# Performance work log

Measured on AMD Instinct MI355X. Metric: run time of the kernel, lower is better.

Reference implementation:

```python
import jax, jax.numpy as jnp
import numpy as np

EMB = 1024
HEADS = 16
RATE = 1.0


def setup_inputs() -> dict:
    key = jax.random.key(0)
    ks = jax.random.split(key, 11)
    B, S, D = 2, 2048, EMB
    s = 1.0 / np.sqrt(D)
    inp = {
        "q": jax.random.normal(ks[0], (B, S, D), jnp.float32),
        "k": jax.random.normal(ks[1], (B, S, D), jnp.float32),
        "v": jax.random.normal(ks[2], (B, S, D), jnp.float32),
        "Wq": jax.random.normal(ks[3], (D, D), jnp.float32) * s,
        "bq": jnp.zeros((D,), jnp.float32),
        "Wk": jax.random.normal(ks[4], (D, D), jnp.float32) * s,
        "bk": jnp.zeros((D,), jnp.float32),
        "Wv": jax.random.normal(ks[5], (D, D), jnp.float32) * s,
        "bv": jnp.zeros((D,), jnp.float32),
        "Wo": jax.random.normal(ks[6], (D, D), jnp.float32) * s,
        "bo": jnp.zeros((D,), jnp.float32),
    }
    return inp


def _mha(q, k, v, Wq, bq, Wk, bk, Wv, bv, Wo, bo):
    B, S, D = q.shape
    H = HEADS
    hd = D // H
    temp = jnp.asarray(hd ** 0.5, q.dtype)

    def proj(x, W, b):
        # nn.Linear: x @ W.T + b, then Scaler: /rate
        y = (jnp.einsum('bsd,ed->bse', x, W) + b) / RATE
        # [B,S,D] -> [B,H,S,hd]
        return y.reshape(B, S, H, hd).transpose(0, 2, 1, 3)

    qh, kh, vh = proj(q, Wq, bq), proj(k, Wk, bk), proj(v, Wv, bv)
    scores = jnp.einsum('bhqd,bhkd->bhqk', qh, kh) / temp  # [B,H,S,S]
    causal = jnp.tril(jnp.ones((S, S), bool))
    scores = jnp.where(causal, scores, jnp.asarray(-jnp.inf, scores.dtype))
    attn = jax.nn.softmax(scores, axis=-1)
    out = jnp.einsum('bhqk,bhkd->bhqd', attn, vh)  # [B,H,S,hd]
    out = out.transpose(0, 2, 1, 3).reshape(B, S, D)
    out = (jnp.einsum('bsd,ed->bse', out, Wo) + bo) / RATE
    # attn returned as [B*H, S, S] to match torch reshape-to-batches layout
    return out, attn.reshape(B * H, S, S)


def reference(q, k, v, Wq, bq, Wk, bk, Wv, bv, Wo, bo):
    return _mha(q, k, v, Wq, bq, Wk, bk, Wv, bv, Wo, bo)
```

## Files before the change

kernel.cpp:

```cpp
#include <hip/hip_runtime.h>
#include <hip/hip_bf16.h>
#include <stdint.h>


#define SLEN 2048
#define DMODEL 1024
#define NBH 32

typedef __bf16 bf16x8 __attribute__((ext_vector_type(8)));
typedef float f32x4 __attribute__((ext_vector_type(4)));
typedef unsigned short us8 __attribute__((ext_vector_type(8)));

__device__ __forceinline__ unsigned short f2bf(float f) {
  union { float f; uint32_t u; } x; x.f = f;
  uint32_t r = x.u + 0x7fffu + ((x.u >> 16) & 1u);
  return (unsigned short)(r >> 16);
}

__device__ __forceinline__ f32x4 mfma16(us8 a, us8 b, f32x4 c) {
  return __builtin_amdgcn_mfma_f32_16x16x32_bf16(
      __builtin_bit_cast(bf16x8, a), __builtin_bit_cast(bf16x8, b), c, 0, 0, 0);
}

__device__ __forceinline__ void gld16(void* lds, const void* g) {
  __builtin_amdgcn_global_load_lds(
      (__attribute__((address_space(1))) void*)(g),
      (__attribute__((address_space(3))) void*)(lds), 16, 0, 0);
}

__device__ __forceinline__ int sw8(int r, int c)  { return (r * 8  + (c ^ (r & 7)))  * 16; }
__device__ __forceinline__ int sw16(int r, int c) { return (r * 16 + (c ^ (r & 15))) * 16; }

__global__ __launch_bounds__(256)
void convert_bf16(const float* __restrict__ q, const float* __restrict__ k,
                  const float* __restrict__ v, const float* __restrict__ wq,
                  const float* __restrict__ wk, const float* __restrict__ wv,
                  const float* __restrict__ wo, unsigned short* __restrict__ dst) {
  size_t i = ((size_t)blockIdx.x * 256 + threadIdx.x) * 8;
  const float* src;
  size_t off;
  if      (i <  4194304u) { src = q;  off = i; }
  else if (i <  8388608u) { src = k;  off = i -  4194304u; }
  else if (i < 12582912u) { src = v;  off = i -  8388608u; }
  else if (i < 13631488u) { src = wq; off = i - 12582912u; }
  else if (i < 14680064u) { src = wk; off = i - 13631488u; }
  else if (i < 15728640u) { src = wv; off = i - 14680064u; }
  else                    { src = wo; off = i - 15728640u; }
  float4 a = *(const float4*)(src + off);
  float4 b = *(const float4*)(src + off + 4);
  us8 u;
  u[0]=f2bf(a.x); u[1]=f2bf(a.y); u[2]=f2bf(a.z); u[3]=f2bf(a.w);
  u[4]=f2bf(b.x); u[5]=f2bf(b.y); u[6]=f2bf(b.z); u[7]=f2bf(b.w);
  *(us8*)(dst + i) = u;
}

__global__ __launch_bounds__(256)
void gemm_qkv_bf(const unsigned short* __restrict__ xq, const unsigned short* __restrict__ xk,
                 const unsigned short* __restrict__ xv, const unsigned short* __restrict__ wwq,
                 const unsigned short* __restrict__ wwk, const unsigned short* __restrict__ wwv,
                 const float* __restrict__ bbq, const float* __restrict__ bbk,
                 const float* __restrict__ bbv,
                 unsigned short* __restrict__ qh, unsigned short* __restrict__ kk,
                 unsigned short* __restrict__ vt) {
  __shared__ __align__(16) unsigned char As[16384];
  __shared__ __align__(16) unsigned char Bs[16384];
  const int p = blockIdx.z;
  const unsigned short* X = (p == 0) ? xq  : (p == 1) ? xk  : xv;
  const unsigned short* W = (p == 0) ? wwq : (p == 1) ? wwk : wwv;
  const float* bias       = (p == 0) ? bbq : (p == 1) ? bbk : bbv;
  const int n0 = blockIdx.x * 128, m0 = blockIdx.y * 128;
  const int t = threadIdx.x, lane = t & 63, w = t >> 6;
  const int quad = lane >> 4, l16 = lane & 15;
  const int wm = w >> 1, wn = w & 1;
  f32x4 acc[4][4] = {};

  for (int kt = 0; kt < 16; ++kt) {
#pragma unroll
    for (int i = 0; i < 4; ++i) {
      int lin = i * 256 + t;
      int r = lin >> 3, cp = lin & 7, c = cp ^ (r & 7);
      gld16(As + lin * 16, X + (size_t)(m0 + r) * DMODEL + kt * 64 + c * 8);
      gld16(Bs + lin * 16, W + (size_t)(n0 + r) * DMODEL + kt * 64 + c * 8);
    }
    __syncthreads();
#pragma unroll
    for (int ks = 0; ks < 2; ++ks) {
      int c = ks * 4 + quad;
      us8 af[4], bf[4];
#pragma unroll
      for (int mt = 0; mt < 4; ++mt) af[mt] = *(const us8*)(As + sw8(wm * 64 + mt * 16 + l16, c));
#pragma unroll
      for (int nt = 0; nt < 4; ++nt) bf[nt] = *(const us8*)(Bs + sw8(wn * 64 + nt * 16 + l16, c));
#pragma unroll
      for (int mt = 0; mt < 4; ++mt)
#pragma unroll
        for (int nt = 0; nt < 4; ++nt)
          acc[mt][nt] = mfma16(af[mt], bf[nt], acc[mt][nt]);
    }
    __syncthreads();
  }
#pragma unroll
  for (int nt = 0; nt < 4; ++nt) {
    int e = n0 + wn * 64 + nt * 16 + l16;
    float bb = bias[e];
    int hh = e >> 6, tt = e & 63;
#pragma unroll
    for (int mt = 0; mt < 4; ++mt) {
#pragma unroll
      for (int rg = 0; rg < 4; ++rg) {
        int row = m0 + wm * 64 + mt * 16 + quad * 4 + rg;
        int b = row >> 11, s = row & 2047;
        unsigned short val = f2bf(acc[mt][nt][rg] + bb);
        int bhh = b * 16 + hh;
        if (p == 0)      qh[(size_t)(bhh * 2048 + s) * 64 + tt] = val;
        else if (p == 1) kk[(size_t)(bhh * 2048 + s) * 64 + tt] = val;
        else             vt[(size_t)(bhh * 64 + tt) * 2048 + s] = val;
      }
    }
  }
}

__global__ __launch_bounds__(256)
void gemm_qkv_f32(const float* __restrict__ xq, const float* __restrict__ xk,
                  const float* __restrict__ xv, const float* __restrict__ wwq,
                  const float* __restrict__ wwk, const float* __restrict__ wwv,
                  const float* __restrict__ bbq, const float* __restrict__ bbk,
                  const float* __restrict__ bbv,
                  unsigned short* __restrict__ qh, unsigned short* __restrict__ kk,
                  unsigned short* __restrict__ vt) {
  __shared__ __align__(16) unsigned char As[16384];
  __shared__ __align__(16) unsigned char Bs[16384];
  const int p = blockIdx.z;
  const float* X    = (p == 0) ? xq  : (p == 1) ? xk  : xv;
  const float* W    = (p == 0) ? wwq : (p == 1) ? wwk : wwv;
  const float* bias = (p == 0) ? bbq : (p == 1) ? bbk : bbv;
  const int n0 = blockIdx.x * 128, m0 = blockIdx.y * 128;
  const int t = threadIdx.x, lane = t & 63, w = t >> 6;
  const int quad = lane >> 4, l16 = lane & 15;
  const int wm = w >> 1, wn = w & 1;
  f32x4 acc[4][4] = {};

  for (int kt = 0; kt < 16; ++kt) {
#pragma unroll
    for (int i = 0; i < 4; ++i) {
      int lin = i * 256 + t;
      int r = lin >> 3, cp = lin & 7, c = cp ^ (r & 7);
      const float* g = X + (size_t)(m0 + r) * DMODEL + kt * 64 + c * 8;
      float4 f0 = *(const float4*)g;
      float4 f1 = *(const float4*)(g + 4);
      us8 u;
      u[0]=f2bf(f0.x); u[1]=f2bf(f0.y); u[2]=f2bf(f0.z); u[3]=f2bf(f0.w);
      u[4]=f2bf(f1.x); u[5]=f2bf(f1.y); u[6]=f2bf(f1.z); u[7]=f2bf(f1.w);
      *(us8*)(As + lin * 16) = u;
      const float* g2 = W + (size_t)(n0 + r) * DMODEL + kt * 64 + c * 8;
      float4 h0 = *(const float4*)g2;
      float4 h1 = *(const float4*)(g2 + 4);
      us8 vv;
      vv[0]=f2bf(h0.x); vv[1]=f2bf(h0.y); vv[2]=f2bf(h0.z); vv[3]=f2bf(h0.w);
      vv[4]=f2bf(h1.x); vv[5]=f2bf(h1.y); vv[6]=f2bf(h1.z); vv[7]=f2bf(h1.w);
      *(us8*)(Bs + lin * 16) = vv;
    }
    __syncthreads();
#pragma unroll
    for (int ks = 0; ks < 2; ++ks) {
      int c = ks * 4 + quad;
      us8 af[4], bf[4];
#pragma unroll
      for (int mt = 0; mt < 4; ++mt) af[mt] = *(const us8*)(As + sw8(wm * 64 + mt * 16 + l16, c));
#pragma unroll
      for (int nt = 0; nt < 4; ++nt) bf[nt] = *(const us8*)(Bs + sw8(wn * 64 + nt * 16 + l16, c));
#pragma unroll
      for (int mt = 0; mt < 4; ++mt)
#pragma unroll
        for (int nt = 0; nt < 4; ++nt)
          acc[mt][nt] = mfma16(af[mt], bf[nt], acc[mt][nt]);
    }
    __syncthreads();
  }
#pragma unroll
  for (int nt = 0; nt < 4; ++nt) {
    int e = n0 + wn * 64 + nt * 16 + l16;
    float bb = bias[e];
    int hh = e >> 6, tt = e & 63;
#pragma unroll
    for (int mt = 0; mt < 4; ++mt) {
#pragma unroll
      for (int rg = 0; rg < 4; ++rg) {
        int row = m0 + wm * 64 + mt * 16 + quad * 4 + rg;
        int b = row >> 11, s = row & 2047;
        unsigned short val = f2bf(acc[mt][nt][rg] + bb);
        int bhh = b * 16 + hh;
        if (p == 0)      qh[(size_t)(bhh * 2048 + s) * 64 + tt] = val;
        else if (p == 1) kk[(size_t)(bhh * 2048 + s) * 64 + tt] = val;
        else             vt[(size_t)(bhh * 64 + tt) * 2048 + s] = val;
      }
    }
  }
}

__global__ __launch_bounds__(256)
void attn_kernel(const unsigned short* __restrict__ qh,
                 const unsigned short* __restrict__ kk,
                 const unsigned short* __restrict__ vt,
                 unsigned short* __restrict__ ctx,
                 float* __restrict__ attn) {
  __shared__ __align__(16) unsigned char Ks[16384];
  __shared__ __align__(16) unsigned char Vts[16384];
  __shared__ __align__(16) unsigned char Ps[16384];
  const int bid = blockIdx.x;
  const int bh = bid >> 4;
  const int qt = (bid < 256) ? (bid & 15) : (15 - (bid & 15));
  const int q0 = qt * 128;
  const int t = threadIdx.x, lane = t & 63, w = t >> 6;
  const int quad = lane >> 4, l16 = lane & 15;
  const size_t bho = (size_t)bh * SLEN * 64;

  us8 qf[2][2];
#pragma unroll
  for (int mq = 0; mq < 2; ++mq)
#pragma unroll
    for (int ks = 0; ks < 2; ++ks)
      qf[mq][ks] = *(const us8*)(qh + bho + (size_t)(q0 + w * 32 + mq * 16 + l16) * 64 + ks * 32 + quad * 8);

  float mrow[2][4], lrow[2][4];
#pragma unroll
  for (int mq = 0; mq < 2; ++mq)
#pragma unroll
    for (int rg = 0; rg < 4; ++rg) { mrow[mq][rg] = -3e38f; lrow[mq][rg] = 0.f; }

  for (int kt = 0; kt <= qt; ++kt) {
    __syncthreads();
#pragma unroll
    for (int i = 0; i < 4; ++i) {
      int lin = i * 256 + t, r = lin >> 3, cp = lin & 7, c = cp ^ (r & 7);
      gld16(Ks + lin * 16, kk + bho + (size_t)(kt * 128 + r) * 64 + c * 8);
    }
    __syncthreads();
    f32x4 sacc[2][8] = {};
#pragma unroll
    for (int ks = 0; ks < 2; ++ks) {
      int c = ks * 4 + quad;
      us8 bfr[8];
#pragma unroll
      for (int nk = 0; nk < 8; ++nk) bfr[nk] = *(const us8*)(Ks + sw8(nk * 16 + l16, c));
#pragma unroll
      for (int mq = 0; mq < 2; ++mq)
#pragma unroll
        for (int nk = 0; nk < 8; ++nk)
          sacc[mq][nk] = mfma16(qf[mq][ks], bfr[nk], sacc[mq][nk]);
    }
    const bool diag = (kt == qt);
#pragma unroll
    for (int mq = 0; mq < 2; ++mq)
#pragma unroll
      for (int rg = 0; rg < 4; ++rg) {
        int qrow = q0 + w * 32 + mq * 16 + quad * 4 + rg;
        float sv[8];
        float pm = -3e38f;
#pragma unroll
        for (int nk = 0; nk < 8; ++nk) {
          float vvv = sacc[mq][nk][rg] * 0.125f;
          if (diag && (kt * 128 + nk * 16 + l16) > qrow) vvv = -3e38f;
          sv[nk] = vvv;
          pm = fmaxf(pm, vvv);
        }
        pm = fmaxf(pm, __shfl_xor(pm, 1));
        pm = fmaxf(pm, __shfl_xor(pm, 2));
        pm = fmaxf(pm, __shfl_xor(pm, 4));
        pm = fmaxf(pm, __shfl_xor(pm, 8));
        float mn = fmaxf(mrow[mq][rg], pm);
        float ps = 0.f;
#pragma unroll
        for (int nk = 0; nk < 8; ++nk) ps += __expf(sv[nk] - mn);
        ps += __shfl_xor(ps, 1);
        ps += __shfl_xor(ps, 2);
        ps += __shfl_xor(ps, 4);
        ps += __shfl_xor(ps, 8);
        lrow[mq][rg] = lrow[mq][rg] * __expf(mrow[mq][rg] - mn) + ps;
        mrow[mq][rg] = mn;
      }
  }
  float rl[2][4];
#pragma unroll
  for (int mq = 0; mq < 2; ++mq)
#pragma unroll
    for (int rg = 0; rg < 4; ++rg) rl[mq][rg] = 1.0f / lrow[mq][rg];

  f32x4 oacc[2][4] = {};
  float* attnb = attn + (size_t)bh * SLEN * SLEN + (size_t)q0 * SLEN;
  for (int kt = 0; kt < 16; ++kt) {
    if (kt <= qt) {
      __syncthreads();
#pragma unroll
      for (int i = 0; i < 4; ++i) {
        int lin = i * 256 + t, r = lin >> 3, cp = lin & 7, c = cp ^ (r & 7);
        gld16(Ks + lin * 16, kk + bho + (size_t)(kt * 128 + r) * 64 + c * 8);
      }
#pragma unroll
      for (int i = 0; i < 4; ++i) {
        int lin = i * 256 + t, r = lin >> 4, cp = lin & 15, c = cp ^ (r & 15);
        gld16(Vts + lin * 16, vt + bho + (size_t)r * SLEN + kt * 128 + c * 8);
      }
      __syncthreads();
      f32x4 sacc[2][8] = {};
#pragma unroll
      for (int ks = 0; ks < 2; ++ks) {
        int c = ks * 4 + quad;
        us8 bfr[8];
#pragma unroll
        for (int nk = 0; nk < 8; ++nk) bfr[nk] = *(const us8*)(Ks + sw8(nk * 16 + l16, c));
#pragma unroll
        for (int mq = 0; mq < 2; ++mq)
#pragma unroll
          for (int nk = 0; nk < 8; ++nk)
            sacc[mq][nk] = mfma16(qf[mq][ks], bfr[nk], sacc[mq][nk]);
      }
      const bool diag = (kt == qt);
#pragma unroll
      for (int mq = 0; mq < 2; ++mq)
#pragma unroll
        for (int nk = 0; nk < 8; ++nk) {
          int col = kt * 128 + nk * 16 + l16;
#pragma unroll
          for (int rg = 0; rg < 4; ++rg) {
            int qrow = q0 + w * 32 + mq * 16 + quad * 4 + rg;
            float vvv = sacc[mq][nk][rg] * 0.125f;
            float p = __expf(vvv - mrow[mq][rg]) * rl[mq][rg];
            if (diag && col > qrow) p = 0.f;
            sacc[mq][nk][rg] = p;
            attnb[(size_t)(w * 32 + mq * 16 + quad * 4 + rg) * SLEN + col] = p;
          }
        }
#pragma unroll
      for (int kh2 = 0; kh2 < 2; ++kh2) {
#pragma unroll
        for (int mq = 0; mq < 2; ++mq)
#pragma unroll
          for (int nkk = 0; nkk < 4; ++nkk) {
            int nk = kh2 * 4 + nkk;
#pragma unroll
            for (int rg = 0; rg < 4; ++rg) {
              int pr = w * 32 + mq * 16 + quad * 4 + rg;
              int kl = nkk * 16 + l16;
              *(unsigned short*)(Ps + (pr * 8 + ((kl >> 3) ^ (pr & 7))) * 16 + (kl & 7) * 2)
                  = f2bf(sacc[mq][nk][rg]);
            }
          }
#pragma unroll
        for (int ks = 0; ks < 2; ++ks) {
          int ca = ks * 4 + quad;
          us8 pa[2];
#pragma unroll
          for (int mq = 0; mq < 2; ++mq)
            pa[mq] = *(const us8*)(Ps + sw8(w * 32 + mq * 16 + l16, ca));
          int cb = kh2 * 8 + ks * 4 + quad;
          us8 vb[4];
#pragma unroll
          for (int nd = 0; nd < 4; ++nd) vb[nd] = *(const us8*)(Vts + sw16(nd * 16 + l16, cb));
#pragma unroll
          for (int mq = 0; mq < 2; ++mq)
#pragma unroll
            for (int nd = 0; nd < 4; ++nd)
              oacc[mq][nd] = mfma16(pa[mq], vb[nd], oacc[mq][nd]);
        }
      }
    } else {
      float4 z = make_float4(0.f, 0.f, 0.f, 0.f);
#pragma unroll
      for (int i = 0; i < 16; ++i) {
        int idx = i * 256 + t, r = idx >> 5, c4 = idx & 31;
        *(float4*)(attnb + (size_t)r * SLEN + kt * 128 + c4 * 4) = z;
      }
    }
  }
  int b = bh >> 4, h = bh & 15;
#pragma unroll
  for (int mq = 0; mq < 2; ++mq)
#pragma unroll
    for (int nd = 0; nd < 4; ++nd)
#pragma unroll
      for (int rg = 0; rg < 4; ++rg) {
        int qrow = q0 + w * 32 + mq * 16 + quad * 4 + rg;
        int e = h * 64 + nd * 16 + l16;
        ctx[(size_t)(b * SLEN + qrow) * DMODEL + e] = f2bf(oacc[mq][nd][rg]);
      }
}

__global__ __launch_bounds__(256)
void gemm_out_bf(const unsigned short* __restrict__ ctx, const unsigned short* __restrict__ wo,
                 const float* __restrict__ bo, float* __restrict__ out) {
  __shared__ __align__(16) unsigned char As[16384];
  __shared__ __align__(16) unsigned char Bs[16384];
  const int n0 = blockIdx.x * 128, m0 = blockIdx.y * 128;
  const int t = threadIdx.x, lane = t & 63, w = t >> 6;
  const int quad = lane >> 4, l16 = lane & 15;
  const int wm = w >> 1, wn = w & 1;
  f32x4 acc[4][4] = {};

  for (int kt = 0; kt < 16; ++kt) {
#pragma unroll
    for (int i = 0; i < 4; ++i) {
      int lin = i * 256 + t;
      int r = lin >> 3, cp = lin & 7, c = cp ^ (r & 7);
      gld16(As + lin * 16, ctx + (size_t)(m0 + r) * DMODEL + kt * 64 + c * 8);
      gld16(Bs + lin * 16, wo  + (size_t)(n0 + r) * DMODEL + kt * 64 + c * 8);
    }
    __syncthreads();
#pragma unroll
    for (int ks = 0; ks < 2; ++ks) {
      int c = ks * 4 + quad;
      us8 af[4], bf[4];
#pragma unroll
      for (int mt = 0; mt < 4; ++mt) af[mt] = *(const us8*)(As + sw8(wm * 64 + mt * 16 + l16, c));
#pragma unroll
      for (int nt = 0; nt < 4; ++nt) bf[nt] = *(const us8*)(Bs + sw8(wn * 64 + nt * 16 + l16, c));
#pragma unroll
      for (int mt = 0; mt < 4; ++mt)
#pragma unroll
        for (int nt = 0; nt < 4; ++nt)
          acc[mt][nt] = mfma16(af[mt], bf[nt], acc[mt][nt]);
    }
    __syncthreads();
  }
#pragma unroll
  for (int nt = 0; nt < 4; ++nt) {
    int e = n0 + wn * 64 + nt * 16 + l16;
    float bb = bo[e];
#pragma unroll
    for (int mt = 0; mt < 4; ++mt)
#pragma unroll
      for (int rg = 0; rg < 4; ++rg) {
        int row = m0 + wm * 64 + mt * 16 + quad * 4 + rg;
        out[(size_t)row * DMODEL + e] = acc[mt][nt][rg] + bb;
      }
  }
}

__global__ __launch_bounds__(256)
void gemm_out_f32(const unsigned short* __restrict__ ctx, const float* __restrict__ wo,
                  const float* __restrict__ bo, float* __restrict__ out) {
  __shared__ __align__(16) unsigned char As[16384];
  __shared__ __align__(16) unsigned char Bs[16384];
  const int n0 = blockIdx.x * 128, m0 = blockIdx.y * 128;
  const int t = threadIdx.x, lane = t & 63, w = t >> 6;
  const int quad = lane >> 4, l16 = lane & 15;
  const int wm = w >> 1, wn = w & 1;
  f32x4 acc[4][4] = {};

  for (int kt = 0; kt < 16; ++kt) {
#pragma unroll
    for (int i = 0; i < 4; ++i) {
      int lin = i * 256 + t;
      int r = lin >> 3, cp = lin & 7, c = cp ^ (r & 7);
      gld16(As + lin * 16, ctx + (size_t)(m0 + r) * DMODEL + kt * 64 + c * 8);
      const float* g2 = wo + (size_t)(n0 + r) * DMODEL + kt * 64 + c * 8;
      float4 h0 = *(const float4*)g2;
      float4 h1 = *(const float4*)(g2 + 4);
      us8 vv;
      vv[0]=f2bf(h0.x); vv[1]=f2bf(h0.y); vv[2]=f2bf(h0.z); vv[3]=f2bf(h0.w);
      vv[4]=f2bf(h1.x); vv[5]=f2bf(h1.y); vv[6]=f2bf(h1.z); vv[7]=f2bf(h1.w);
      *(us8*)(Bs + lin * 16) = vv;
    }
    __syncthreads();
#pragma unroll
    for (int ks = 0; ks < 2; ++ks) {
      int c = ks * 4 + quad;
      us8 af[4], bf[4];
#pragma unroll
      for (int mt = 0; mt < 4; ++mt) af[mt] = *(const us8*)(As + sw8(wm * 64 + mt * 16 + l16, c));
#pragma unroll
      for (int nt = 0; nt < 4; ++nt) bf[nt] = *(const us8*)(Bs + sw8(wn * 64 + nt * 16 + l16, c));
#pragma unroll
      for (int mt = 0; mt < 4; ++mt)
#pragma unroll
        for (int nt = 0; nt < 4; ++nt)
          acc[mt][nt] = mfma16(af[mt], bf[nt], acc[mt][nt]);
    }
    __syncthreads();
  }
#pragma unroll
  for (int nt = 0; nt < 4; ++nt) {
    int e = n0 + wn * 64 + nt * 16 + l16;
    float bb = bo[e];
#pragma unroll
    for (int mt = 0; mt < 4; ++mt)
#pragma unroll
      for (int rg = 0; rg < 4; ++rg) {
        int row = m0 + wm * 64 + mt * 16 + quad * 4 + rg;
        out[(size_t)row * DMODEL + e] = acc[mt][nt][rg] + bb;
      }
  }
}

extern "C" void kernel_launch(void* const* d_in, const int* in_sizes, int n_in,
                              void* d_out, int out_size, void* d_ws, size_t ws_size,
                              hipStream_t stream) {
  const float* q  = (const float*)d_in[0];
  const float* k  = (const float*)d_in[1];
  const float* v  = (const float*)d_in[2];
  const float* Wq = (const float*)d_in[3];
  const float* bq = (const float*)d_in[4];
  const float* Wk = (const float*)d_in[5];
  const float* bk = (const float*)d_in[6];
  const float* Wv = (const float*)d_in[7];
  const float* bv = (const float*)d_in[8];
  const float* Wo = (const float*)d_in[9];
  const float* bo = (const float*)d_in[10];
  float* out  = (float*)d_out;
  float* attn = out + (size_t)2 * SLEN * DMODEL;

  unsigned short* qh  = (unsigned short*)d_ws;
  unsigned short* kh  = qh  + (size_t)4194304;
  unsigned short* vt  = kh  + (size_t)4194304;
  unsigned short* ctx = vt  + (size_t)4194304;
  unsigned short* xbq = ctx + (size_t)4194304;
  unsigned short* xbk = xbq + (size_t)4194304;
  unsigned short* xbv = xbk + (size_t)4194304;
  unsigned short* wbq = xbv + (size_t)4194304;
  unsigned short* wbk = wbq + (size_t)1048576;
  unsigned short* wbv = wbk + (size_t)1048576;
  unsigned short* wbo = wbv + (size_t)1048576;

  const size_t WS_FULL = (size_t)67108864;

  if (ws_size >= WS_FULL) {
    convert_bf16<<<8192, 256, 0, stream>>>(q, k, v, Wq, Wk, Wv, Wo, xbq);
    gemm_qkv_bf<<<dim3(8, 32, 3), 256, 0, stream>>>(xbq, xbk, xbv, wbq, wbk, wbv,
                                                    bq, bk, bv, qh, kh, vt);
    attn_kernel<<<512, 256, 0, stream>>>(qh, kh, vt, ctx, attn);
    gemm_out_bf<<<dim3(8, 32), 256, 0, stream>>>(ctx, wbo, bo, out);
  } else {
    gemm_qkv_f32<<<dim3(8, 32, 3), 256, 0, stream>>>(q, k, v, Wq, Wk, Wv,
                                                     bq, bk, bv, qh, kh, vt);
    attn_kernel<<<512, 256, 0, stream>>>(qh, kh, vt, ctx, attn);
    gemm_out_f32<<<dim3(8, 32), 256, 0, stream>>>(ctx, Wo, bo, out);
  }
}
```

Measured before the change: 794.0 us.

## Double-buffer K/V tiles in attention and reuse the K buffer for P

```diff
diff --git a/kernel.cpp b/kernel.cpp
--- a/kernel.cpp
+++ b/kernel.cpp
@@ -26,6 +26,13 @@
   __builtin_amdgcn_global_load_lds(
       (__attribute__((address_space(1))) void*)(g),
       (__attribute__((address_space(3))) void*)(lds), 16, 0, 0);
+}
+
+__device__ __forceinline__ void barrier_lgkm_only() {
+  asm volatile("s_waitcnt lgkmcnt(0)" ::: "memory");
+  __builtin_amdgcn_sched_barrier(0);
+  __builtin_amdgcn_s_barrier();
+  __builtin_amdgcn_sched_barrier(0);
 }
 
 __device__ __forceinline__ int sw8(int r, int c)  { return (r * 8  + (c ^ (r & 7)))  * 16; }
@@ -204,9 +211,8 @@
                  const unsigned short* __restrict__ vt,
                  unsigned short* __restrict__ ctx,
                  float* __restrict__ attn) {
-  __shared__ __align__(16) unsigned char Ks[16384];
-  __shared__ __align__(16) unsigned char Vts[16384];
-  __shared__ __align__(16) unsigned char Ps[16384];
+  __shared__ __align__(16) unsigned char Ks[2][16384];
+  __shared__ __align__(16) unsigned char Vts[2][16384];
   const int bid = blockIdx.x;
   const int bh = bid >> 4;
   const int qt = (bid < 256) ? (bid & 15) : (15 - (bid & 15));
@@ -215,6 +221,21 @@
   const int quad = lane >> 4, l16 = lane & 15;
   const size_t bho = (size_t)bh * SLEN * 64;
 
+  auto stageK = [&](int buf, int kt) {
+#pragma unroll
+    for (int i = 0; i < 4; ++i) {
+      int lin = i * 256 + t, r = lin >> 3, cp = lin & 7, c = cp ^ (r & 7);
+      gld16(Ks[buf] + lin * 16, kk + bho + (size_t)(kt * 128 + r) * 64 + c * 8);
+    }
+  };
+  auto stageV = [&](int buf, int kt) {
+#pragma unroll
+    for (int i = 0; i < 4; ++i) {
+      int lin = i * 256 + t, r = lin >> 4, cp = lin & 15, c = cp ^ (r & 15);
+      gld16(Vts[buf] + lin * 16, vt + bho + (size_t)r * SLEN + kt * 128 + c * 8);
+    }
+  };
+
   us8 qf[2][2];
 #pragma unroll
   for (int mq = 0; mq < 2; ++mq)
@@ -228,21 +249,18 @@
 #pragma unroll
     for (int rg = 0; rg < 4; ++rg) { mrow[mq][rg] = -3e38f; lrow[mq][rg] = 0.f; }
 
+  stageK(0, 0);
   for (int kt = 0; kt <= qt; ++kt) {
-    __syncthreads();
-#pragma unroll
-    for (int i = 0; i < 4; ++i) {
-      int lin = i * 256 + t, r = lin >> 3, cp = lin & 7, c = cp ^ (r & 7);
-      gld16(Ks + lin * 16, kk + bho + (size_t)(kt * 128 + r) * 64 + c * 8);
-    }
-    __syncthreads();
+    const int cur = kt & 1;
+    __syncthreads();
+    if (kt < qt) stageK(cur ^ 1, kt + 1);
     f32x4 sacc[2][8] = {};
 #pragma unroll
     for (int ks = 0; ks < 2; ++ks) {
       int c = ks * 4 + quad;
       us8 bfr[8];
 #pragma unroll
-      for (int nk = 0; nk < 8; ++nk) bfr[nk] = *(const us8*)(Ks + sw8(nk * 16 + l16, c));
+      for (int nk = 0; nk < 8; ++nk) bfr[nk] = *(const us8*)(Ks[cur] + sw8(nk * 16 + l16, c));
 #pragma unroll
       for (int mq = 0; mq < 2; ++mq)
 #pragma unroll
@@ -288,89 +306,84 @@
 
   f32x4 oacc[2][4] = {};
   float* attnb = attn + (size_t)bh * SLEN * SLEN + (size_t)q0 * SLEN;
-  for (int kt = 0; kt < 16; ++kt) {
-    if (kt <= qt) {
-      __syncthreads();
-#pragma unroll
-      for (int i = 0; i < 4; ++i) {
-        int lin = i * 256 + t, r = lin >> 3, cp = lin & 7, c = cp ^ (r & 7);
-        gld16(Ks + lin * 16, kk + bho + (size_t)(kt * 128 + r) * 64 + c * 8);
-      }
-#pragma unroll
-      for (int i = 0; i < 4; ++i) {
-        int lin = i * 256 + t, r = lin >> 4, cp = lin & 15, c = cp ^ (r & 15);
-        gld16(Vts + lin * 16, vt + bho + (size_t)r * SLEN + kt * 128 + c * 8);
-      }
-      __syncthreads();
-      f32x4 sacc[2][8] = {};
-#pragma unroll
-      for (int ks = 0; ks < 2; ++ks) {
-        int c = ks * 4 + quad;
-        us8 bfr[8];
-#pragma unroll
-        for (int nk = 0; nk < 8; ++nk) bfr[nk] = *(const us8*)(Ks + sw8(nk * 16 + l16, c));
-#pragma unroll
-        for (int mq = 0; mq < 2; ++mq)
-#pragma unroll
-          for (int nk = 0; nk < 8; ++nk)
-            sacc[mq][nk] = mfma16(qf[mq][ks], bfr[nk], sacc[mq][nk]);
-      }
-      const bool diag = (kt == qt);
+  __syncthreads();
+  stageK(0, 0);
+  stageV(0, 0);
+  for (int kt = 0; kt <= qt; ++kt) {
+    const int cur = kt & 1;
+    __syncthreads();
+    if (kt < qt) { stageK(cur ^ 1, kt + 1); stageV(cur ^ 1, kt + 1); }
+    f32x4 sacc[2][8] = {};
+#pragma unroll
+    for (int ks = 0; ks < 2; ++ks) {
+      int c = ks * 4 + quad;
+      us8 bfr[8];
+#pragma unroll
+      for (int nk = 0; nk < 8; ++nk) bfr[nk] = *(const us8*)(Ks[cur] + sw8(nk * 16 + l16, c));
 #pragma unroll
       for (int mq = 0; mq < 2; ++mq)
 #pragma unroll
-        for (int nk = 0; nk < 8; ++nk) {
-          int col = kt * 128 + nk * 16 + l16;
+        for (int nk = 0; nk < 8; ++nk)
+          sacc[mq][nk] = mfma16(qf[mq][ks], bfr[nk], sacc[mq][nk]);
+    }
+    const bool diag = (kt == qt);
+#pragma unroll
+    for (int mq = 0; mq < 2; ++mq)
+#pragma unroll
+      for (int nk = 0; nk < 8; ++nk) {
+        int col = kt * 128 + nk * 16 + l16;
+#pragma unroll
+        for (int rg = 0; rg < 4; ++rg) {
+          int qrow = q0 + w * 32 + mq * 16 + quad * 4 + rg;
+          float vvv = sacc[mq][nk][rg] * 0.125f;
+          float p = __expf(vvv - mrow[mq][rg]) * rl[mq][rg];
+          if (diag && col > qrow) p = 0.f;
+          sacc[mq][nk][rg] = p;
+          attnb[(size_t)(w * 32 + mq * 16 + quad * 4 + rg) * SLEN + col] = p;
+        }
+      }
+    barrier_lgkm_only();
+    unsigned char* Pb = Ks[cur];
+#pragma unroll
+    for (int kh2 = 0; kh2 < 2; ++kh2) {
+#pragma unroll
+      for (int mq = 0; mq < 2; ++mq)
+#pragma unroll
+        for (int nkk = 0; nkk < 4; ++nkk) {
+          int nk = kh2 * 4 + nkk;
 #pragma unroll
           for (int rg = 0; rg < 4; ++rg) {
-            int qrow = q0 + w * 32 + mq * 16 + quad * 4 + rg;
-            float vvv = sacc[mq][nk][rg] * 0.125f;
-            float p = __expf(vvv - mrow[mq][rg]) * rl[mq][rg];
-            if (diag && col > qrow) p = 0.f;
-            sacc[mq][nk][rg] = p;
-            attnb[(size_t)(w * 32 + mq * 16 + quad * 4 + rg) * SLEN + col] = p;
+            int pr = w * 32 + mq * 16 + quad * 4 + rg;
+            int kl = nkk * 16 + l16;
+            *(unsigned short*)(Pb + (pr * 8 + ((kl >> 3) ^ (pr & 7))) * 16 + (kl & 7) * 2)
+                = f2bf(sacc[mq][nk][rg]);
           }
         }
 #pragma unroll
-      for (int kh2 = 0; kh2 < 2; ++kh2) {
+      for (int ks = 0; ks < 2; ++ks) {
+        int ca = ks * 4 + quad;
+        us8 pa[2];
 #pragma unroll
         for (int mq = 0; mq < 2; ++mq)
-#pragma unroll
-          for (int nkk = 0; nkk < 4; ++nkk) {
-            int nk = kh2 * 4 + nkk;
-#pragma unroll
-            for (int rg = 0; rg < 4; ++rg) {
-              int pr = w * 32 + mq * 16 + quad * 4 + rg;
-              int kl = nkk * 16 + l16;
-              *(unsigned short*)(Ps + (pr * 8 + ((kl >> 3) ^ (pr & 7))) * 16 + (kl & 7) * 2)
-                  = f2bf(sacc[mq][nk][rg]);
-            }
-          }
-#pragma unroll
-        for (int ks = 0; ks < 2; ++ks) {
-          int ca = ks * 4 + quad;
-          us8 pa[2];
-#pragma unroll
-          for (int mq = 0; mq < 2; ++mq)
-            pa[mq] = *(const us8*)(Ps + sw8(w * 32 + mq * 16 + l16, ca));
-          int cb = kh2 * 8 + ks * 4 + quad;
-          us8 vb[4];
-#pragma unroll
-          for (int nd = 0; nd < 4; ++nd) vb[nd] = *(const us8*)(Vts + sw16(nd * 16 + l16, cb));
-#pragma unroll
-          for (int mq = 0; mq < 2; ++mq)
-#pragma unroll
-            for (int nd = 0; nd < 4; ++nd)
-              oacc[mq][nd] = mfma16(pa[mq], vb[nd], oacc[mq][nd]);
-        }
-      }
-    } else {
-      float4 z = make_float4(0.f, 0.f, 0.f, 0.f);
-#pragma unroll
-      for (int i = 0; i < 16; ++i) {
-        int idx = i * 256 + t, r = idx >> 5, c4 = idx & 31;
-        *(float4*)(attnb + (size_t)r * SLEN + kt * 128 + c4 * 4) = z;
-      }
+          pa[mq] = *(const us8*)(Pb + sw8(w * 32 + mq * 16 + l16, ca));
+        int cb = kh2 * 8 + ks * 4 + quad;
+        us8 vb[4];
+#pragma unroll
+        for (int nd = 0; nd < 4; ++nd) vb[nd] = *(const us8*)(Vts[cur] + sw16(nd * 16 + l16, cb));
+#pragma unroll
+        for (int mq = 0; mq < 2; ++mq)
+#pragma unroll
+          for (int nd = 0; nd < 4; ++nd)
+            oacc[mq][nd] = mfma16(pa[mq], vb[nd], oacc[mq][nd]);
+      }
+    }
+  }
+  for (int kt = qt + 1; kt < 16; ++kt) {
+    float4 z = make_float4(0.f, 0.f, 0.f, 0.f);
+#pragma unroll
+    for (int i = 0; i < 16; ++i) {
+      int idx = i * 256 + t, r = idx >> 5, c4 = idx & 31;
+      *(float4*)(attnb + (size_t)r * SLEN + kt * 128 + c4 * 4) = z;
     }
   }
   int b = bh >> 4, h = bh & 15;
```

New measurement: 806.7 us. No clear change (+1.6%).
